# Optimization experiments

Hardware: AMD Instinct MI355X
Metric: run time of the kernel (lower is better)

## Reference

```python
import jax, jax.numpy as jnp
import numpy as np

D_MODEL = 2048
N_HEADS = 16
HEAD_DIM = D_MODEL // N_HEADS  # 128
ROPE_THETA = 10000.0
BATCH = 2
SEQ_LEN = 2048  # == window_size -> dense causal SDPA path


def setup_inputs() -> dict:
    key = jax.random.key(0)
    ks = jax.random.split(key, 5)
    scale = 1.0 / np.sqrt(D_MODEL)
    x = jax.random.normal(ks[0], (BATCH, SEQ_LEN, D_MODEL), dtype=jnp.float32)
    # torch nn.Linear weights are stored (out_features, in_features); y = x @ W.T
    Wq = jax.random.normal(ks[1], (D_MODEL, D_MODEL), dtype=jnp.float32) * scale
    Wk = jax.random.normal(ks[2], (D_MODEL, D_MODEL), dtype=jnp.float32) * scale
    Wv = jax.random.normal(ks[3], (D_MODEL, D_MODEL), dtype=jnp.float32) * scale
    Wo = jax.random.normal(ks[4], (D_MODEL, D_MODEL), dtype=jnp.float32) * scale
    return {"x": x, "Wq": Wq, "Wk": Wk, "Wv": Wv, "Wo": Wo}


def _apply_rope(x):
    # x: [B, H, S, HEAD_DIM]; interleaved-pair RoPE, positions 0..S-1
    S = x.shape[2]
    inv_freq = 1.0 / (ROPE_THETA ** (jnp.arange(0, HEAD_DIM, 2, dtype=jnp.float32) / HEAD_DIM))
    t = jnp.arange(S, dtype=jnp.float32)
    freqs = jnp.outer(t, inv_freq)            # [S, HEAD_DIM//2]
    cos = jnp.cos(freqs)
    sin = jnp.sin(freqs)
    x1 = x[..., 0::2]
    x2 = x[..., 1::2]
    rot = jnp.stack([x1 * cos - x2 * sin, x1 * sin + x2 * cos], axis=-1)  # [B,H,S,hd/2,2]
    return rot.reshape(x.shape)


def reference(x, Wq, Wk, Wv, Wo):
    B, S, _ = x.shape
    q = (x @ Wq.T).reshape(B, S, N_HEADS, HEAD_DIM).transpose(0, 2, 1, 3)  # [B,H,S,D]
    k = (x @ Wk.T).reshape(B, S, N_HEADS, HEAD_DIM).transpose(0, 2, 1, 3)
    v = (x @ Wv.T).reshape(B, S, N_HEADS, HEAD_DIM).transpose(0, 2, 1, 3)
    q = _apply_rope(q)
    k = _apply_rope(k)
    scores = jnp.einsum("bhqd,bhkd->bhqk", q, k) / np.sqrt(HEAD_DIM).astype(np.float32)
    causal = jnp.tril(jnp.ones((S, S), dtype=bool))
    scores = jnp.where(causal, scores, -jnp.inf)
    attn = jax.nn.softmax(scores, axis=-1)
    out = jnp.einsum("bhqk,bhkd->bhqd", attn, v)
    out = out.transpose(0, 2, 1, 3).reshape(B, S, N_HEADS * HEAD_DIM)
    return out @ Wo.T
```

## Files before the change

### kernel.cpp

```cpp
#include <hip/hip_runtime.h>
#include <stdint.h>

#define D_MODEL 2048
#define SEQ     2048
#define BATCH   2
#define NHEAD   16
#define HD      128
#define MROWS   (BATCH*SEQ)

typedef short short8 __attribute__((ext_vector_type(8)));
typedef float f32x4  __attribute__((ext_vector_type(4)));

__device__ __forceinline__ unsigned short f2b(float f) {
  unsigned int u = __float_as_uint(f);
  u += 0x7fffu + ((u >> 16) & 1u);
  return (unsigned short)(u >> 16);
}
__device__ __forceinline__ float b2f(unsigned short s) {
  return __uint_as_float(((unsigned int)s) << 16);
}
__device__ __forceinline__ void gll16(const void* g, void* l) {
  __builtin_amdgcn_global_load_lds((const __attribute__((address_space(1))) void*)g,
                                   (__attribute__((address_space(3))) void*)l, 16, 0, 0);
}
__device__ __forceinline__ void barrier_nodrain() {
  asm volatile("" ::: "memory");
  __builtin_amdgcn_s_barrier();
  asm volatile("" ::: "memory");
}
template<int N> __device__ __forceinline__ void vmwait() {
  if constexpr (N == 0)      asm volatile("s_waitcnt vmcnt(0)" ::: "memory");
  else if constexpr (N == 1) asm volatile("s_waitcnt vmcnt(1)" ::: "memory");
  else if constexpr (N == 2) asm volatile("s_waitcnt vmcnt(2)" ::: "memory");
  else if constexpr (N == 3) asm volatile("s_waitcnt vmcnt(3)" ::: "memory");
  else if constexpr (N == 4) asm volatile("s_waitcnt vmcnt(4)" ::: "memory");
  else if constexpr (N == 5) asm volatile("s_waitcnt vmcnt(5)" ::: "memory");
  else if constexpr (N == 6) asm volatile("s_waitcnt vmcnt(6)" ::: "memory");
  else if constexpr (N == 7) asm volatile("s_waitcnt vmcnt(7)" ::: "memory");
  else                       asm volatile("s_waitcnt vmcnt(8)" ::: "memory");
}

__global__ __launch_bounds__(256) void cast_all(
    const float* __restrict__ x,  const float* __restrict__ Wq,
    const float* __restrict__ Wk, const float* __restrict__ Wv,
    const float* __restrict__ Wo, unsigned short* __restrict__ dst)
{
  size_t e = ((size_t)blockIdx.x * 256 + threadIdx.x) * 4;
  const size_t XN = (size_t)MROWS * D_MODEL;
  const size_t WN = (size_t)D_MODEL * D_MODEL;
  const float* src; size_t off;
  if (e < XN) { src = x; off = e; }
  else {
    size_t e2 = e - XN;
    int w = (int)(e2 >> 22);
    off = e2 & (WN - 1);
    src = (w == 0) ? Wq : (w == 1) ? Wk : (w == 2) ? Wv : Wo;
  }
  float4 v = *(const float4*)(src + off);
  ushort4 o;
  o.x = f2b(v.x); o.y = f2b(v.y); o.z = f2b(v.z); o.w = f2b(v.w);
  *(ushort4*)(dst + e) = o;
}

template<int BM, int LA>
__device__ __forceinline__ void gemm_8ph(
    const unsigned short* __restrict__ A, const unsigned short* __restrict__ Bw,
    unsigned short* __restrict__ As, unsigned short* __restrict__ Bs,
    int m0, int n0, int tid, f32x4 (&acc)[BM / 32][4])
{
  constexpr int K = D_MODEL, NT = K / 64;
  constexpr int HA = BM / 2;
  constexpr int MI = BM / 32, MIH = MI / 2;
  constexpr int AHALF = HA * 64;
  constexpr int BHALF = 128 * 64;
  constexpr int P2N = 2 * (LA + 2);
  constexpr int P4N = 2 * LA + 2;
  const int wave = tid >> 6, lane = tid & 63, l15 = lane & 15, quad = lane >> 4;
  const int wr = wave >> 2, wc = wave & 3;
  const int rA = wr * 16 + l15;
  const int rB = wc * 16 + l15;
  const int swk = l15 & 7;

  auto stA = [&](int buf, int h, int t) {
    #pragma unroll
    for (int i = 0; i < LA; ++i) {
      int slot = i * 512 + tid, rw = slot >> 3, ch = slot & 7;
      gll16(A + (size_t)(m0 + h * HA + rw) * K + t * 64 + ((ch ^ (rw & 7)) * 8),
            As + (buf * 2 + h) * AHALF + (i * 512 + wave * 64) * 8);
    }
  };
  auto stB = [&](int buf, int h, int t) {
    #pragma unroll
    for (int i = 0; i < 2; ++i) {
      int slot = i * 512 + tid, rw = slot >> 3, ch = slot & 7;
      gll16(Bw + (size_t)(n0 + h * 128 + rw) * K + t * 64 + ((ch ^ (rw & 7)) * 8),
            Bs + (buf * 2 + h) * BHALF + (i * 512 + wave * 64) * 8);
    }
  };
  auto ldA = [&](int buf, int h, int ml, int ks) -> short8 {
    int rw = ml * 32 + rA;
    return *(const short8*)(As + (buf * 2 + h) * AHALF + rw * 64 + (((ks * 4 + quad) ^ swk) * 8));
  };
  auto ldB = [&](int buf, int h, int nl, int ks) -> short8 {
    int rw = nl * 64 + rB;
    return *(const short8*)(Bs + (buf * 2 + h) * BHALF + rw * 64 + (((ks * 4 + quad) ^ swk) * 8));
  };

  stA(0, 0, 0); stB(0, 0, 0); stA(0, 1, 0); stB(0, 1, 0);
  stA(1, 0, 1); stB(1, 1, 1);
  vmwait<LA + 2>();
  barrier_nodrain();

  short8 ah[MIH][2], b0[2][2], b1[2][2];

  #pragma unroll 1
  for (int t = 0; t < NT; ++t) {
    const int buf = t & 1;

    #pragma unroll
    for (int ml = 0; ml < MIH; ++ml) {
      ah[ml][0] = ldA(buf, 0, ml, 0); ah[ml][1] = ldA(buf, 0, ml, 1);
    }
    #pragma unroll
    for (int nl = 0; nl < 2; ++nl) {
      b0[nl][0] = ldB(buf, 0, nl, 0); b0[nl][1] = ldB(buf, 0, nl, 1);
    }
    if (t + 1 < NT) stB(buf ^ 1, 0, t + 1);
    barrier_nodrain();
    asm volatile("s_waitcnt lgkmcnt(0)" ::: "memory");
    __builtin_amdgcn_sched_barrier(0);
    __builtin_amdgcn_s_setprio(1);
    #pragma unroll
    for (int ml = 0; ml < MIH; ++ml)
      #pragma unroll
      for (int nl = 0; nl < 2; ++nl)
        #pragma unroll
        for (int ks = 0; ks < 2; ++ks)
          acc[ml][nl] = __builtin_amdgcn_mfma_f32_16x16x32_bf16(ah[ml][ks], b0[nl][ks], acc[ml][nl], 0, 0, 0);
    __builtin_amdgcn_s_setprio(0);
    barrier_nodrain();

    #pragma unroll
    for (int nl = 0; nl < 2; ++nl) {
      b1[nl][0] = ldB(buf, 1, nl, 0); b1[nl][1] = ldB(buf, 1, nl, 1);
    }
    if (t + 1 < NT) stA(buf ^ 1, 1, t + 1);
    if (t == NT - 1) vmwait<0>(); else vmwait<P2N>();
    barrier_nodrain();
    asm volatile("s_waitcnt lgkmcnt(0)" ::: "memory");
    __builtin_amdgcn_sched_barrier(0);
    __builtin_amdgcn_s_setprio(1);
    #pragma unroll
    for (int ml = 0; ml < MIH; ++ml)
      #pragma unroll
      for (int nl = 0; nl < 2; ++nl)
        #pragma unroll
        for (int ks = 0; ks < 2; ++ks)
          acc[ml][2 + nl] = __builtin_amdgcn_mfma_f32_16x16x32_bf16(ah[ml][ks], b1[nl][ks], acc[ml][2 + nl], 0, 0, 0);
    __builtin_amdgcn_s_setprio(0);
    barrier_nodrain();

    #pragma unroll
    for (int ml = 0; ml < MIH; ++ml) {
      ah[ml][0] = ldA(buf, 1, ml, 0); ah[ml][1] = ldA(buf, 1, ml, 1);
    }
    if (t + 2 < NT) stA(buf, 0, t + 2);
    barrier_nodrain();
    asm volatile("s_waitcnt lgkmcnt(0)" ::: "memory");
    __builtin_amdgcn_sched_barrier(0);
    __builtin_amdgcn_s_setprio(1);
    #pragma unroll
    for (int ml = 0; ml < MIH; ++ml)
      #pragma unroll
      for (int nl = 0; nl < 2; ++nl)
        #pragma unroll
        for (int ks = 0; ks < 2; ++ks)
          acc[MIH + ml][2 + nl] = __builtin_amdgcn_mfma_f32_16x16x32_bf16(ah[ml][ks], b1[nl][ks], acc[MIH + ml][2 + nl], 0, 0, 0);
    __builtin_amdgcn_s_setprio(0);
    barrier_nodrain();

    if (t + 2 < NT) stB(buf, 1, t + 2);
    if (t < NT - 1) { if (t == NT - 2) vmwait<LA>(); else vmwait<P4N>(); }
    barrier_nodrain();
    __builtin_amdgcn_s_setprio(1);
    #pragma unroll
    for (int ml = 0; ml < MIH; ++ml)
      #pragma unroll
      for (int nl = 0; nl < 2; ++nl)
        #pragma unroll
        for (int ks = 0; ks < 2; ++ks)
          acc[MIH + ml][nl] = __builtin_amdgcn_mfma_f32_16x16x32_bf16(ah[ml][ks], b0[nl][ks], acc[MIH + ml][nl], 0, 0, 0);
    __builtin_amdgcn_s_setprio(0);
    barrier_nodrain();
  }
}

template<int BM, int BN>
__device__ __forceinline__ void gemm_pipe(
    const unsigned short* __restrict__ A, const unsigned short* __restrict__ Bw,
    unsigned short* __restrict__ As, unsigned short* __restrict__ Bs,
    int m0, int n0, int tid, f32x4 (&acc)[BM / 32][4])
{
  constexpr int K  = D_MODEL;
  constexpr int NT = K / 64;
  constexpr int LA = BM / 64, LB = BN / 64;
  constexpr int LT = LA + LB;
  constexpr int MI = BM / 32, MH = MI / 2;
  const int wave = tid >> 6, lane = tid & 63, l15 = lane & 15, quad = lane >> 4;
  const int wr = wave >> 2, wc = wave & 3;
  const int sw = l15 & 7;
  const int arow = wr * (BM / 2) + l15;
  const int brow = wc * (BN / 4) + l15;

  auto stage = [&](int buf, int t) {
    const int kt = t * 64;
    #pragma unroll
    for (int i = 0; i < LA; ++i) {
      int slot = i * 512 + tid;
      int row = slot >> 3, ch = slot & 7;
      gll16(A + (size_t)(m0 + row) * K + kt + ((ch ^ (row & 7)) * 8),
            As + (size_t)buf * (BM * 64) + (size_t)(i * 512 + wave * 64) * 8);
    }
    #pragma unroll
    for (int i = 0; i < LB; ++i) {
      int slot = i * 512 + tid;
      int row = slot >> 3, ch = slot & 7;
      gll16(Bw + (size_t)(n0 + row) * K + kt + ((ch ^ (row & 7)) * 8),
            Bs + (size_t)buf * (BN * 64) + (size_t)(i * 512 + wave * 64) * 8);
    }
  };

  stage(0, 0);
  stage(1, 1);

  short8 ah[MH][2], bf[4][2];

  #pragma unroll 1
  for (int t = 0; t < NT; ++t) {
    const int cur = t & 1;
    if (t < NT - 1) {
      if constexpr (LT == 8) vmwait<8>(); else vmwait<6>();
    } else {
      vmwait<0>();
    }
    barrier_nodrain();

    const unsigned short* as = As + cur * (BM * 64);
    const unsigned short* bs = Bs + cur * (BN * 64);

    #pragma unroll
    for (int mi = 0; mi < MH; ++mi)
      #pragma unroll
      for (int ks = 0; ks < 2; ++ks)
        ah[mi][ks] = *(const short8*)(as + (arow + mi * 16) * 64 + (((ks * 4 + quad) ^ sw) * 8));
    #pragma unroll
    for (int ni = 0; ni < 2; ++ni)
      #pragma unroll
      for (int ks = 0; ks < 2; ++ks)
        bf[ni][ks] = *(const short8*)(bs + (brow + ni * 16) * 64 + (((ks * 4 + quad) ^ sw) * 8));
    __builtin_amdgcn_s_setprio(1);
    #pragma unroll
    for (int mi = 0; mi < MH; ++mi)
      #pragma unroll
      for (int ni = 0; ni < 2; ++ni)
        #pragma unroll
        for (int ks = 0; ks < 2; ++ks)
          acc[mi][ni] = __builtin_amdgcn_mfma_f32_16x16x32_bf16(ah[mi][ks], bf[ni][ks], acc[mi][ni], 0, 0, 0);
    __builtin_amdgcn_s_setprio(0);

    #pragma unroll
    for (int ni = 2; ni < 4; ++ni)
      #pragma unroll
      for (int ks = 0; ks < 2; ++ks)
        bf[ni][ks] = *(const short8*)(bs + (brow + ni * 16) * 64 + (((ks * 4 + quad) ^ sw) * 8));
    __builtin_amdgcn_s_setprio(1);
    #pragma unroll
    for (int mi = 0; mi < MH; ++mi)
      #pragma unroll
      for (int ni = 2; ni < 4; ++ni)
        #pragma unroll
        for (int ks = 0; ks < 2; ++ks)
          acc[mi][ni] = __builtin_amdgcn_mfma_f32_16x16x32_bf16(ah[mi][ks], bf[ni][ks], acc[mi][ni], 0, 0, 0);
    __builtin_amdgcn_s_setprio(0);

    #pragma unroll
    for (int mi = 0; mi < MH; ++mi)
      #pragma unroll
      for (int ks = 0; ks < 2; ++ks)
        ah[mi][ks] = *(const short8*)(as + (arow + (mi + MH) * 16) * 64 + (((ks * 4 + quad) ^ sw) * 8));
    __builtin_amdgcn_s_setprio(1);
    #pragma unroll
    for (int mi = 0; mi < MH; ++mi)
      #pragma unroll
      for (int ni = 2; ni < 4; ++ni)
        #pragma unroll
        for (int ks = 0; ks < 2; ++ks)
          acc[mi + MH][ni] = __builtin_amdgcn_mfma_f32_16x16x32_bf16(ah[mi][ks], bf[ni][ks], acc[mi + MH][ni], 0, 0, 0);
    #pragma unroll
    for (int mi = 0; mi < MH; ++mi)
      #pragma unroll
      for (int ni = 0; ni < 2; ++ni)
        #pragma unroll
        for (int ks = 0; ks < 2; ++ks)
          acc[mi + MH][ni] = __builtin_amdgcn_mfma_f32_16x16x32_bf16(ah[mi][ks], bf[ni][ks], acc[mi + MH][ni], 0, 0, 0);
    __builtin_amdgcn_s_setprio(0);

    barrier_nodrain();
    if (t + 2 < NT) stage(cur, t + 2);
  }
}

__global__ __launch_bounds__(512, 2) void gemm_qkv3(
    const unsigned short* __restrict__ Axb, const unsigned short* __restrict__ Wqkv,
    unsigned short* __restrict__ Qh, unsigned short* __restrict__ Kh,
    unsigned short* __restrict__ Vt)
{
  __shared__ unsigned short As[2 * 2 * 128 * 64];
  __shared__ unsigned short Bs[2 * 2 * 128 * 64];
  const int hw  = blockIdx.y * 24 + blockIdx.x;
  const int swz = (hw & 7) * 48 + (hw >> 3);
  const int m0  = (swz & 15) * 256;
  const int n0g = (swz >> 4) * 256;
  f32x4 acc[8][4];
  #pragma unroll
  for (int i = 0; i < 8; ++i)
    #pragma unroll
    for (int j = 0; j < 4; ++j) acc[i][j] = (f32x4){0.f, 0.f, 0.f, 0.f};

  gemm_8ph<256, 2>(Axb, Wqkv, As, Bs, m0, n0g, threadIdx.x, acc);

  const int tid = threadIdx.x, wave = tid >> 6, lane = tid & 63;
  const int l15 = lane & 15, quad = lane >> 4, wr = wave >> 2, wc = wave & 3;
  const int z = n0g >> 11;
  if (z < 2) {
    unsigned short* dst = z ? Kh : Qh;
    #pragma unroll
    for (int mi = 0; mi < 8; ++mi)
      #pragma unroll
      for (int ni = 0; ni < 4; ++ni) {
        int row0 = m0 + mi * 32 + wr * 16 + quad * 4;
        int col  = (n0g + ni * 64 + wc * 16 + l15) & (D_MODEL - 1);
        int h = col >> 7, d = col & (HD - 1);
        #pragma unroll
        for (int r = 0; r < 4; ++r) {
          int m = row0 + r; int bb = m >> 11; int s = m & (SEQ - 1);
          dst[((size_t)(bb * NHEAD + h) * SEQ + s) * HD + d] = f2b(acc[mi][ni][r]);
        }
      }
  } else {
    #pragma unroll
    for (int mi = 0; mi < 8; ++mi)
      #pragma unroll
      for (int ni = 0; ni < 4; ++ni) {
        int row0 = m0 + mi * 32 + wr * 16 + quad * 4;
        int col  = (n0g + ni * 64 + wc * 16 + l15) & (D_MODEL - 1);
        int h = col >> 7, d = col & (HD - 1);
        int bb = row0 >> 11; int s = row0 & (SEQ - 1);
        ushort4 pk;
        pk.x = f2b(acc[mi][ni][0]); pk.y = f2b(acc[mi][ni][1]);
        pk.z = f2b(acc[mi][ni][2]); pk.w = f2b(acc[mi][ni][3]);
        *(ushort4*)(Vt + ((size_t)(bb * NHEAD + h) * HD + d) * SEQ + s) = pk;
      }
  }
}

__global__ __launch_bounds__(512, 2) void gemm_out2(
    const unsigned short* __restrict__ A, const unsigned short* __restrict__ Wo,
    float* __restrict__ C)
{
  __shared__ unsigned short As[2 * 128 * 64];
  __shared__ unsigned short Bs[2 * 256 * 64];
  const int hw  = blockIdx.y * 8 + blockIdx.x;
  const int swz = (hw & 7) * 32 + (hw >> 3);
  const int m0  = (swz & 31) * 128;
  const int n0  = (swz >> 5) * 256;
  f32x4 acc[4][4];
  #pragma unroll
  for (int i = 0; i < 4; ++i)
    #pragma unroll
    for (int j = 0; j < 4; ++j) acc[i][j] = (f32x4){0.f, 0.f, 0.f, 0.f};

  gemm_pipe<128, 256>(A, Wo, As, Bs, m0, n0, threadIdx.x, acc);

  const int tid = threadIdx.x, wave = tid >> 6, lane = tid & 63;
  const int l15 = lane & 15, quad = lane >> 4, wr = wave >> 2, wc = wave & 3;
  #pragma unroll
  for (int mi = 0; mi < 4; ++mi)
    #pragma unroll
    for (int ni = 0; ni < 4; ++ni) {
      int row0 = m0 + wr * 64 + mi * 16 + quad * 4;
      int col  = n0 + wc * 64 + ni * 16 + l15;
      #pragma unroll
      for (int r = 0; r < 4; ++r)
        C[(size_t)(row0 + r) * D_MODEL + col] = acc[mi][ni][r];
    }
}

__global__ __launch_bounds__(256) void rope_k(unsigned short* __restrict__ Qh,
                                              unsigned short* __restrict__ Kh)
{
  unsigned short* P = blockIdx.y ? Kh : Qh;
  int rid = blockIdx.x * 4 + (threadIdx.x >> 6);
  int i = threadIdx.x & 63;
  int s = rid & (SEQ - 1);
  size_t base = (size_t)rid * HD + 2 * i;
  float inv = exp2f(-(float)i * (13.287712379549449f / 64.0f));
  float ang = (float)s * inv;
  float sn, cs; sincosf(ang, &sn, &cs);
  unsigned int pk = *(const unsigned int*)(P + base);
  float x1 = b2f((unsigned short)(pk & 0xffffu));
  float x2 = b2f((unsigned short)(pk >> 16));
  unsigned short o0 = f2b(x1 * cs - x2 * sn);
  unsigned short o1 = f2b(x1 * sn + x2 * cs);
  *(unsigned int*)(P + base) = (unsigned int)o0 | ((unsigned int)o1 << 16);
}

__global__ __launch_bounds__(256) void attn_k2(
    const unsigned short* __restrict__ Qh, const unsigned short* __restrict__ Kh,
    const unsigned short* __restrict__ Vt, unsigned short* __restrict__ Aout)
{
  __shared__ unsigned short Ks[2][64 * 128];
  __shared__ unsigned short Vs[2][128 * 64];
  __shared__ unsigned short sPb[4][16 * 72];
  const int tid = threadIdx.x;
  const int wave = tid >> 6, lane = tid & 63, l15 = lane & 15, quad = lane >> 4;
  const int bh = blockIdx.y;
  const int b = bh >> 4, h = bh & 15;
  const unsigned short* Qb = Qh + (size_t)bh * SEQ * HD;
  const unsigned short* Kb = Kh + (size_t)bh * SEQ * HD;
  const unsigned short* Vb = Vt + (size_t)bh * HD * SEQ;
  unsigned short* pw = &sPb[wave][0];
  const float scl = 0.08838834764831845f * 1.4426950408889634f;

  auto stageKV = [&](int bsel, int it) {
    const int k0 = it * 64;
    unsigned short* kd = &Ks[bsel][0];
    unsigned short* vd = &Vs[bsel][0];
    #pragma unroll
    for (int c = 0; c < 4; ++c) {
      int slot = c * 256 + tid;
      int kr = slot >> 4, pch = slot & 15;
      gll16(Kb + (size_t)(k0 + kr) * HD + ((pch ^ (kr & 15)) * 8), kd + slot * 8);
    }
    #pragma unroll
    for (int c = 0; c < 4; ++c) {
      int slot = c * 256 + tid;
      int vr = slot >> 3, pch = slot & 7;
      gll16(Vb + (size_t)vr * SEQ + k0 + ((pch ^ (vr & 7)) * 8), vd + slot * 8);
    }
  };

  #pragma unroll
  for (int half = 0; half < 2; ++half) {
    const int tile = half ? (31 - blockIdx.x) : blockIdx.x;
    const int q0w = tile * 64 + wave * 16;
    const int q = q0w + l15;

    short8 qf[4];
    #pragma unroll
    for (int c = 0; c < 4; ++c)
      qf[c] = *(const short8*)(Qb + (size_t)(q0w + l15) * HD + c * 32 + quad * 8);

    f32x4 o[8];
    #pragma unroll
    for (int dj = 0; dj < 8; ++dj) o[dj] = (f32x4){0.f, 0.f, 0.f, 0.f};
    float ms = -1e30f, ls = 0.f;

    const int trips = tile + 1;
    stageKV(0, 0);
    vmwait<0>(); barrier_nodrain();

    for (int it = 0; it < trips; ++it) {
      const int cb = it & 1;
      const int k0 = it * 64;
      if (it + 1 < trips) stageKV(cb ^ 1, it + 1);

      const unsigned short* KsB = &Ks[cb][0];
      const unsigned short* VsB = &Vs[cb][0];

      f32x4 st[4];
      #pragma unroll
      for (int ni = 0; ni < 4; ++ni) st[ni] = (f32x4){0.f, 0.f, 0.f, 0.f};
      __builtin_amdgcn_s_setprio(1);
      #pragma unroll
      for (int ni = 0; ni < 4; ++ni) {
        const int rowb = (ni * 16 + l15) * 128;
        #pragma unroll
        for (int c = 0; c < 4; ++c) {
          short8 kf = *(const short8*)(KsB + rowb + (((c * 4 + quad) ^ l15) * 8));
          st[ni] = __builtin_amdgcn_mfma_f32_16x16x32_bf16(kf, qf[c], st[ni], 0, 0, 0);
        }
      }
      __builtin_amdgcn_s_setprio(0);

      if (k0 + 63 > q0w) {
        #pragma unroll
        for (int ni = 0; ni < 4; ++ni)
          #pragma unroll
          for (int r = 0; r < 4; ++r) {
            int k = k0 + ni * 16 + quad * 4 + r;
            if (k > q) st[ni][r] = -1e30f;
          }
      }

      float lm = -1e30f;
      #pragma unroll
      for (int ni = 0; ni < 4; ++ni)
        #pragma unroll
        for (int r = 0; r < 4; ++r) lm = fmaxf(lm, st[ni][r]);
      lm = fmaxf(lm, __shfl_xor(lm, 16, 64));
      lm = fmaxf(lm, __shfl_xor(lm, 32, 64));
      float mn = fmaxf(ms, lm);
      float al = exp2f((ms - mn) * scl);
      ms = mn;
      float nm = mn * scl;
      float rs = 0.f;
      #pragma unroll
      for (int ni = 0; ni < 4; ++ni)
        #pragma unroll
        for (int r = 0; r < 4; ++r) {
          float p = exp2f(fmaf(st[ni][r], scl, -nm));
          st[ni][r] = p;
          rs += p;
        }
      rs += __shfl_xor(rs, 16, 64);
      rs += __shfl_xor(rs, 32, 64);
      ls = ls * al + rs;
      #pragma unroll
      for (int dj = 0; dj < 8; ++dj) o[dj] *= al;

      #pragma unroll
      for (int ni = 0; ni < 4; ++ni) {
        ushort4 pk;
        pk.x = f2b(st[ni][0]); pk.y = f2b(st[ni][1]);
        pk.z = f2b(st[ni][2]); pk.w = f2b(st[ni][3]);
        *(ushort4*)(pw + l15 * 72 + ni * 16 + quad * 4) = pk;
      }
      short8 pf0 = *(const short8*)(pw + l15 * 72 + quad * 8);
      short8 pf1 = *(const short8*)(pw + l15 * 72 + 32 + quad * 8);

      __builtin_amdgcn_s_setprio(1);
      #pragma unroll
      for (int dj = 0; dj < 8; ++dj) {
        const int vrow = (dj * 16 + l15) * 64;
        short8 v0 = *(const short8*)(VsB + vrow + (((quad) ^ (l15 & 7)) * 8));
        short8 v1 = *(const short8*)(VsB + vrow + (((4 + quad) ^ (l15 & 7)) * 8));
        o[dj] = __builtin_amdgcn_mfma_f32_16x16x32_bf16(v0, pf0, o[dj], 0, 0, 0);
        o[dj] = __builtin_amdgcn_mfma_f32_16x16x32_bf16(v1, pf1, o[dj], 0, 0, 0);
      }
      __builtin_amdgcn_s_setprio(0);

      vmwait<0>();
      barrier_nodrain();
    }

    float rl = 1.0f / ls;
    #pragma unroll
    for (int dj = 0; dj < 8; ++dj) {
      ushort4 pk;
      pk.x = f2b(o[dj][0] * rl); pk.y = f2b(o[dj][1] * rl);
      pk.z = f2b(o[dj][2] * rl); pk.w = f2b(o[dj][3] * rl);
      *(ushort4*)(Aout + ((size_t)(b * SEQ + q)) * D_MODEL + h * HD + dj * 16 + quad * 4) = pk;
    }
  }
}

extern "C" void kernel_launch(void* const* d_in, const int* in_sizes, int n_in,
                              void* d_out, int out_size, void* d_ws, size_t ws_size,
                              hipStream_t stream)
{
  const float* x  = (const float*)d_in[0];
  const float* Wq = (const float*)d_in[1];
  const float* Wk = (const float*)d_in[2];
  const float* Wv = (const float*)d_in[3];
  const float* Wo = (const float*)d_in[4];
  float* out = (float*)d_out;

  unsigned short* xb  = (unsigned short*)d_ws;
  unsigned short* wqb = xb  + 8388608;
  unsigned short* wkb = wqb + 4194304;
  unsigned short* wvb = wkb + 4194304;
  unsigned short* wob = wvb + 4194304;
  unsigned short* qh  = wob + 4194304;
  unsigned short* kh  = qh  + 8388608;
  unsigned short* vt  = kh  + 8388608;
  unsigned short* ao  = vt  + 8388608;

  (void)wkb; (void)wvb;
  cast_all<<<24576, 256, 0, stream>>>(x, Wq, Wk, Wv, Wo, xb);
  gemm_qkv3<<<dim3(24, 16), 512, 0, stream>>>(xb, wqb, qh, kh, vt);
  rope_k<<<dim3(16384, 2), 256, 0, stream>>>(qh, kh);
  attn_k2<<<dim3(16, 32), 256, 0, stream>>>(qh, kh, vt, ao);
  gemm_out2<<<dim3(8, 32), 512, 0, stream>>>(ao, wob, out);
}
```

Baseline: 407.4 us.

## Restructure QKV GEMM pipeline from eight phases to two and drop block swizzle

The QKV projection GEMM mainloop moves from an 8-phase schedule with four barriers per k-step to a 2-phase schedule. Each phase loads the fragments it needs, issues two stage loads for a later k-step, and runs twice as many MFMAs between barriers. The vmcnt waits are recomputed to match the new issue order. Both GEMM kernels also replace the XCD-aware block-index swizzle with a plain blockIdx mapping, which may change L2 locality across chiplets.

```diff
diff --git a/kernel.cpp b/kernel.cpp
--- a/kernel.cpp
+++ b/kernel.cpp
@@ -29,15 +29,17 @@
   asm volatile("" ::: "memory");
 }
 template<int N> __device__ __forceinline__ void vmwait() {
-  if constexpr (N == 0)      asm volatile("s_waitcnt vmcnt(0)" ::: "memory");
-  else if constexpr (N == 1) asm volatile("s_waitcnt vmcnt(1)" ::: "memory");
-  else if constexpr (N == 2) asm volatile("s_waitcnt vmcnt(2)" ::: "memory");
-  else if constexpr (N == 3) asm volatile("s_waitcnt vmcnt(3)" ::: "memory");
-  else if constexpr (N == 4) asm volatile("s_waitcnt vmcnt(4)" ::: "memory");
-  else if constexpr (N == 5) asm volatile("s_waitcnt vmcnt(5)" ::: "memory");
-  else if constexpr (N == 6) asm volatile("s_waitcnt vmcnt(6)" ::: "memory");
-  else if constexpr (N == 7) asm volatile("s_waitcnt vmcnt(7)" ::: "memory");
-  else                       asm volatile("s_waitcnt vmcnt(8)" ::: "memory");
+  if constexpr (N == 0)       asm volatile("s_waitcnt vmcnt(0)" ::: "memory");
+  else if constexpr (N == 1)  asm volatile("s_waitcnt vmcnt(1)" ::: "memory");
+  else if constexpr (N == 2)  asm volatile("s_waitcnt vmcnt(2)" ::: "memory");
+  else if constexpr (N == 3)  asm volatile("s_waitcnt vmcnt(3)" ::: "memory");
+  else if constexpr (N == 4)  asm volatile("s_waitcnt vmcnt(4)" ::: "memory");
+  else if constexpr (N == 5)  asm volatile("s_waitcnt vmcnt(5)" ::: "memory");
+  else if constexpr (N == 6)  asm volatile("s_waitcnt vmcnt(6)" ::: "memory");
+  else if constexpr (N == 7)  asm volatile("s_waitcnt vmcnt(7)" ::: "memory");
+  else if constexpr (N == 8)  asm volatile("s_waitcnt vmcnt(8)" ::: "memory");
+  else if constexpr (N == 10) asm volatile("s_waitcnt vmcnt(10)" ::: "memory");
+  else                        asm volatile("s_waitcnt vmcnt(12)" ::: "memory");
 }
 
 __global__ __launch_bounds__(256) void cast_all(
@@ -63,7 +65,7 @@
 }
 
 template<int BM, int LA>
-__device__ __forceinline__ void gemm_8ph(
+__device__ __forceinline__ void gemm_2mp(
     const unsigned short* __restrict__ A, const unsigned short* __restrict__ Bw,
     unsigned short* __restrict__ As, unsigned short* __restrict__ Bs,
     int m0, int n0, int tid, f32x4 (&acc)[BM / 32][4])
@@ -73,8 +75,8 @@
   constexpr int MI = BM / 32, MIH = MI / 2;
   constexpr int AHALF = HA * 64;
   constexpr int BHALF = 128 * 64;
-  constexpr int P2N = 2 * (LA + 2);
-  constexpr int P4N = 2 * LA + 2;
+  constexpr int W1 = 2 * LA + 2;
+  constexpr int W2 = 2 * LA + 4;
   const int wave = tid >> 6, lane = tid & 63, l15 = lane & 15, quad = lane >> 4;
   const int wr = wave >> 2, wc = wave & 3;
   const int rA = wr * 16 + l15;
@@ -106,10 +108,9 @@
     return *(const short8*)(Bs + (buf * 2 + h) * BHALF + rw * 64 + (((ks * 4 + quad) ^ swk) * 8));
   };
 
-  stA(0, 0, 0); stB(0, 0, 0); stA(0, 1, 0); stB(0, 1, 0);
+  stA(0, 0, 0); stB(0, 1, 0);
+  stB(0, 0, 0); stA(0, 1, 0);
   stA(1, 0, 1); stB(1, 1, 1);
-  vmwait<LA + 2>();
-  barrier_nodrain();
 
   short8 ah[MIH][2], b0[2][2], b1[2][2];
 
@@ -117,6 +118,8 @@
   for (int t = 0; t < NT; ++t) {
     const int buf = t & 1;
 
+    if (t == NT - 1) vmwait<LA>(); else vmwait<W1>();
+    barrier_nodrain();
     #pragma unroll
     for (int ml = 0; ml < MIH; ++ml) {
       ah[ml][0] = ldA(buf, 0, ml, 0); ah[ml][1] = ldA(buf, 0, ml, 1);
@@ -124,9 +127,9 @@
     #pragma unroll
     for (int nl = 0; nl < 2; ++nl) {
       b0[nl][0] = ldB(buf, 0, nl, 0); b0[nl][1] = ldB(buf, 0, nl, 1);
-    }
-    if (t + 1 < NT) stB(buf ^ 1, 0, t + 1);
-    barrier_nodrain();
+      b1[nl][0] = ldB(buf, 1, nl, 0); b1[nl][1] = ldB(buf, 1, nl, 1);
+    }
+    if (t + 1 < NT) { stB(buf ^ 1, 0, t + 1); stA(buf ^ 1, 1, t + 1); }
     asm volatile("s_waitcnt lgkmcnt(0)" ::: "memory");
     __builtin_amdgcn_sched_barrier(0);
     __builtin_amdgcn_s_setprio(1);
@@ -137,16 +140,22 @@
         #pragma unroll
         for (int ks = 0; ks < 2; ++ks)
           acc[ml][nl] = __builtin_amdgcn_mfma_f32_16x16x32_bf16(ah[ml][ks], b0[nl][ks], acc[ml][nl], 0, 0, 0);
+    #pragma unroll
+    for (int ml = 0; ml < MIH; ++ml)
+      #pragma unroll
+      for (int nl = 0; nl < 2; ++nl)
+        #pragma unroll
+        for (int ks = 0; ks < 2; ++ks)
+          acc[ml][2 + nl] = __builtin_amdgcn_mfma_f32_16x16x32_bf16(ah[ml][ks], b1[nl][ks], acc[ml][2 + nl], 0, 0, 0);
     __builtin_amdgcn_s_setprio(0);
+
+    if (t == NT - 1) vmwait<0>(); else vmwait<W2>();
     barrier_nodrain();
-
-    #pragma unroll
-    for (int nl = 0; nl < 2; ++nl) {
-      b1[nl][0] = ldB(buf, 1, nl, 0); b1[nl][1] = ldB(buf, 1, nl, 1);
-    }
-    if (t + 1 < NT) stA(buf ^ 1, 1, t + 1);
-    if (t == NT - 1) vmwait<0>(); else vmwait<P2N>();
-    barrier_nodrain();
+    #pragma unroll
+    for (int ml = 0; ml < MIH; ++ml) {
+      ah[ml][0] = ldA(buf, 1, ml, 0); ah[ml][1] = ldA(buf, 1, ml, 1);
+    }
+    if (t + 2 < NT) { stA(buf, 0, t + 2); stB(buf, 1, t + 2); }
     asm volatile("s_waitcnt lgkmcnt(0)" ::: "memory");
     __builtin_amdgcn_sched_barrier(0);
     __builtin_amdgcn_s_setprio(1);
@@ -156,33 +165,7 @@
       for (int nl = 0; nl < 2; ++nl)
         #pragma unroll
         for (int ks = 0; ks < 2; ++ks)
-          acc[ml][2 + nl] = __builtin_amdgcn_mfma_f32_16x16x32_bf16(ah[ml][ks], b1[nl][ks], acc[ml][2 + nl], 0, 0, 0);
-    __builtin_amdgcn_s_setprio(0);
-    barrier_nodrain();
-
-    #pragma unroll
-    for (int ml = 0; ml < MIH; ++ml) {
-      ah[ml][0] = ldA(buf, 1, ml, 0); ah[ml][1] = ldA(buf, 1, ml, 1);
-    }
-    if (t + 2 < NT) stA(buf, 0, t + 2);
-    barrier_nodrain();
-    asm volatile("s_waitcnt lgkmcnt(0)" ::: "memory");
-    __builtin_amdgcn_sched_barrier(0);
-    __builtin_amdgcn_s_setprio(1);
-    #pragma unroll
-    for (int ml = 0; ml < MIH; ++ml)
-      #pragma unroll
-      for (int nl = 0; nl < 2; ++nl)
-        #pragma unroll
-        for (int ks = 0; ks < 2; ++ks)
           acc[MIH + ml][2 + nl] = __builtin_amdgcn_mfma_f32_16x16x32_bf16(ah[ml][ks], b1[nl][ks], acc[MIH + ml][2 + nl], 0, 0, 0);
-    __builtin_amdgcn_s_setprio(0);
-    barrier_nodrain();
-
-    if (t + 2 < NT) stB(buf, 1, t + 2);
-    if (t < NT - 1) { if (t == NT - 2) vmwait<LA>(); else vmwait<P4N>(); }
-    barrier_nodrain();
-    __builtin_amdgcn_s_setprio(1);
     #pragma unroll
     for (int ml = 0; ml < MIH; ++ml)
       #pragma unroll
@@ -191,7 +174,6 @@
         for (int ks = 0; ks < 2; ++ks)
           acc[MIH + ml][nl] = __builtin_amdgcn_mfma_f32_16x16x32_bf16(ah[ml][ks], b0[nl][ks], acc[MIH + ml][nl], 0, 0, 0);
     __builtin_amdgcn_s_setprio(0);
-    barrier_nodrain();
   }
 }
 
@@ -317,17 +299,14 @@
 {
   __shared__ unsigned short As[2 * 2 * 128 * 64];
   __shared__ unsigned short Bs[2 * 2 * 128 * 64];
-  const int hw  = blockIdx.y * 24 + blockIdx.x;
-  const int swz = (hw & 7) * 48 + (hw >> 3);
-  const int m0  = (swz & 15) * 256;
-  const int n0g = (swz >> 4) * 256;
+  const int m0 = blockIdx.y * 256, n0g = blockIdx.x * 256;
   f32x4 acc[8][4];
   #pragma unroll
   for (int i = 0; i < 8; ++i)
     #pragma unroll
     for (int j = 0; j < 4; ++j) acc[i][j] = (f32x4){0.f, 0.f, 0.f, 0.f};
 
-  gemm_8ph<256, 2>(Axb, Wqkv, As, Bs, m0, n0g, threadIdx.x, acc);
+  gemm_2mp<256, 2>(Axb, Wqkv, As, Bs, m0, n0g, threadIdx.x, acc);
 
   const int tid = threadIdx.x, wave = tid >> 6, lane = tid & 63;
   const int l15 = lane & 15, quad = lane >> 4, wr = wave >> 2, wc = wave & 3;
@@ -370,10 +349,7 @@
 {
   __shared__ unsigned short As[2 * 128 * 64];
   __shared__ unsigned short Bs[2 * 256 * 64];
-  const int hw  = blockIdx.y * 8 + blockIdx.x;
-  const int swz = (hw & 7) * 32 + (hw >> 3);
-  const int m0  = (swz & 31) * 128;
-  const int n0  = (swz >> 5) * 256;
+  const int m0 = blockIdx.y * 128, n0 = blockIdx.x * 256;
   f32x4 acc[4][4];
   #pragma unroll
   for (int i = 0; i < 4; ++i)
```

Measured after the change: 391.2 us. -4.0%, faster.
